# Performance work log

Hardware: AMD Instinct MI355X
Metric: run time of the kernel (lower is better)

Reference implementation:

```python
import jax, jax.numpy as jnp
import numpy as np

N_NODES = 50000
N_EDGES = 800000
IN_FEATS = 128
HIDDEN = 128
OUT_LEN = 128


def setup_inputs() -> dict:
    key = jax.random.key(0)
    ks = jax.random.split(key, 8)
    feat = jax.random.normal(ks[0], (N_NODES, IN_FEATS), dtype=jnp.float32)
    # Glorot-ish init for weights, zeros for bias (DGL GraphConv default)
    def w(k, fi, fo):
        return jax.random.normal(k, (fi, fo), dtype=jnp.float32) / np.sqrt(fi)
    W1 = w(ks[1], IN_FEATS, HIDDEN)
    W2 = w(ks[2], HIDDEN, HIDDEN)
    W3 = w(ks[3], HIDDEN, OUT_LEN)
    b1 = jnp.zeros((HIDDEN,), jnp.float32)
    b2 = jnp.zeros((HIDDEN,), jnp.float32)
    b3 = jnp.zeros((OUT_LEN,), jnp.float32)
    src = jax.random.randint(ks[4], (N_EDGES,), 0, N_NODES, dtype=jnp.int32)
    dst = jax.random.randint(ks[5], (N_EDGES,), 0, N_NODES, dtype=jnp.int32)
    return {"feat": feat, "W1": W1, "b1": b1, "W2": W2, "b2": b2,
            "W3": W3, "b3": b3, "src": src, "dst": dst}


def _degree_norm(idx, n):
    # degree counts, clamped to min 1 (DGL behavior), then ^{-1/2}
    deg = jax.ops.segment_sum(jnp.ones_like(idx, dtype=jnp.float32), idx,
                              num_segments=n)
    return jax.lax.rsqrt(jnp.maximum(deg, 1.0))


def _graph_conv(x, W, b, src, dst, out_norm, in_norm):
    # DGL GraphConv, norm='both':
    # h = D_dst^{-1/2} * segsum_dst( D_src^{-1/2} * x[src] ) @ W + b
    h = x * out_norm[:, None]
    m = jax.ops.segment_sum(h[src], dst, num_segments=x.shape[0])  # [N, d]
    m = m * in_norm[:, None]
    return m @ W + b


def reference(feat, W1, b1, W2, b2, W3, b3, src, dst):
    out_norm = _degree_norm(src, feat.shape[0])  # out-degree norm (source)
    in_norm = _degree_norm(dst, feat.shape[0])   # in-degree norm (dest)
    h = jax.nn.relu(_graph_conv(feat, W1, b1, src, dst, out_norm, in_norm))
    h = jax.nn.relu(_graph_conv(h, W2, b2, src, dst, out_norm, in_norm))
    h = _graph_conv(h, W3, b3, src, dst, out_norm, in_norm)
    # single graph: mean_nodes == mean over all nodes, then squeeze -> [out_len]
    return jnp.mean(h, axis=0)
```

## Files before the change

### kernel.cpp

```cpp
#include <hip/hip_runtime.h>

#define N_NODES 50000
#define N_EDGES 800000
#define F 128
#define SCAN_NB 49
#define CH 64
#define EPC (N_EDGES / CH)
#define HALF 25000
#define QTR 12500
#define BSTRIDE 17
#define AGG_NB (N_NODES / 4)
#define RED_NB 256

typedef __bf16 bf16x8 __attribute__((ext_vector_type(8)));
typedef float  f32x4  __attribute__((ext_vector_type(4)));
typedef float  f32x2  __attribute__((ext_vector_type(2)));

__device__ inline unsigned short f2bf(float f) {
    unsigned u = __float_as_uint(f);
    u += 0x7FFF + ((u >> 16) & 1);
    return (unsigned short)(u >> 16);
}
__device__ inline unsigned packbf2(float a, float b) {
    return (unsigned)f2bf(a) | ((unsigned)f2bf(b) << 16);
}

__device__ inline void fp8x8_to_f32(uint2 u, float* f) {
    f32x2 v0 = __builtin_amdgcn_cvt_pk_f32_fp8(u.x, false);
    f32x2 v1 = __builtin_amdgcn_cvt_pk_f32_fp8(u.x, true);
    f32x2 v2 = __builtin_amdgcn_cvt_pk_f32_fp8(u.y, false);
    f32x2 v3 = __builtin_amdgcn_cvt_pk_f32_fp8(u.y, true);
    f[0] = v0.x; f[1] = v0.y; f[2] = v1.x; f[3] = v1.y;
    f[4] = v2.x; f[5] = v2.y; f[6] = v3.x; f[7] = v3.y;
}
__device__ inline unsigned f32x4_to_fp8(float a, float b, float c, float d) {
    unsigned r = __builtin_amdgcn_cvt_pk_fp8_f32(a, b, 0, false);
    r = __builtin_amdgcn_cvt_pk_fp8_f32(c, d, r, true);
    return r;
}

__global__ __launch_bounds__(1024) void hist_kernel(const int* __restrict__ src,
                                                    const int* __restrict__ dst,
                                                    unsigned short* __restrict__ Hs16,
                                                    unsigned short* __restrict__ Hd16) {
    __shared__ unsigned hist[HALF / 2];
    int bx = blockIdx.x;
    int c = bx >> 2, t = bx & 1, h = (bx >> 1) & 1;
    const int* ids = t ? dst : src;
    unsigned short* H = t ? Hd16 : Hs16;
    int base = h * HALF;
    for (int j = threadIdx.x; j < HALF / 2; j += 1024) hist[j] = 0;
    __syncthreads();
    int e0 = c * EPC;
    for (int e = e0 + threadIdx.x; e < e0 + EPC; e += 1024) {
        int id = ids[e] - base;
        if ((unsigned)id < (unsigned)HALF)
            atomicAdd(&hist[id >> 1], 1u << ((id & 1) * 16));
    }
    __syncthreads();
    for (int j = threadIdx.x; j < HALF / 2; j += 1024)
        *(unsigned*)&H[(size_t)c * N_NODES + base + 2 * j] = hist[j];
}

__global__ __launch_bounds__(1024) void reduceN_kernel(const unsigned short* __restrict__ Hs16,
                                                       const unsigned short* __restrict__ Hd16,
                                                       float* __restrict__ onorm,
                                                       float* __restrict__ inorm,
                                                       int* __restrict__ degd,
                                                       int* __restrict__ bsums) {
    __shared__ int wsum[16];
    int i = blockIdx.x * 1024 + threadIdx.x;
    int dd = 0;
    if (i < N_NODES) {
        int ds = 0;
        for (int c = 0; c < CH; c++) {
            ds += Hs16[(size_t)c * N_NODES + i];
            dd += Hd16[(size_t)c * N_NODES + i];
        }
        onorm[i] = rsqrtf(fmaxf((float)ds, 1.0f));
        inorm[i] = rsqrtf(fmaxf((float)dd, 1.0f));
        degd[i] = dd;
    }
    int v = dd;
#pragma unroll
    for (int off = 32; off; off >>= 1) v += __shfl_down(v, off);
    if ((threadIdx.x & 63) == 0) wsum[threadIdx.x >> 6] = v;
    __syncthreads();
    if (threadIdx.x == 0) {
        int s = 0;
#pragma unroll
        for (int k = 0; k < 16; k++) s += wsum[k];
        bsums[blockIdx.x] = s;
    }
}

__global__ __launch_bounds__(64) void scanB_kernel(const int* __restrict__ blockSums,
                                                   int* __restrict__ blockOffs) {
    int t = threadIdx.x;
    int v = (t < SCAN_NB) ? blockSums[t] : 0;
    int incl = v;
#pragma unroll
    for (int off = 1; off < 64; off <<= 1) {
        int u = __shfl_up(incl, off);
        if (t >= off) incl += u;
    }
    if (t < SCAN_NB) blockOffs[t] = incl - v;
}

__global__ __launch_bounds__(1024) void tq_kernel(const int* __restrict__ src,
                                                  const int* __restrict__ dst,
                                                  const float* __restrict__ inorm,
                                                  float* __restrict__ Tq) {
    __shared__ float a[QTR];
    int bx = blockIdx.x;
    int c = bx >> 2, q = bx & 3;
    int base = q * QTR;
    for (int j = threadIdx.x; j < QTR; j += 1024) a[j] = 0.0f;
    __syncthreads();
    int e0 = c * EPC;
    for (int e = e0 + threadIdx.x; e < e0 + EPC; e += 1024) {
        int s = src[e] - base;
        if ((unsigned)s < (unsigned)QTR)
            atomicAdd(&a[s], inorm[dst[e]]);
    }
    __syncthreads();
    for (int j = threadIdx.x; j < QTR; j += 1024)
        Tq[(size_t)c * N_NODES + base + j] = a[j];
}

__global__ __launch_bounds__(1024) void scanC_kernel(const int* __restrict__ deg,
                                                     const int* __restrict__ blockOffs,
                                                     int* __restrict__ rowst,
                                                     const unsigned short* __restrict__ Hd16,
                                                     int* __restrict__ P,
                                                     const float* __restrict__ Tq,
                                                     float* __restrict__ qt) {
    __shared__ int wsum[16];
    int t = threadIdx.x, lane = t & 63, w = t >> 6;
    int i = blockIdx.x * 1024 + t;
    int v = (i < N_NODES) ? deg[i] : 0;
    int incl = v;
#pragma unroll
    for (int off = 1; off < 64; off <<= 1) {
        int u = __shfl_up(incl, off);
        if (lane >= off) incl += u;
    }
    if (lane == 63) wsum[w] = incl;
    __syncthreads();
    if (t == 0) {
        int s = 0;
#pragma unroll
        for (int k = 0; k < 16; k++) { int x = wsum[k]; wsum[k] = s; s += x; }
    }
    __syncthreads();
    incl += wsum[w] + blockOffs[blockIdx.x];
    if (i < N_NODES) {
        int s = incl - v;
        rowst[i] = s;
        if (i == N_NODES - 1) rowst[N_NODES] = incl;
        float tsum = 0.0f;
        for (int c = 0; c < CH; c++) {
            size_t o = (size_t)c * N_NODES + i;
            P[o] = s; s += Hd16[o];
            tsum += Tq[o];
        }
        qt[i] = tsum;
    }
}

__global__ __launch_bounds__(1024) void scatter2_kernel(const int* __restrict__ src,
                                                        const int* __restrict__ dst,
                                                        const int* __restrict__ P,
                                                        int* __restrict__ esrc) {
    __shared__ int cur[QTR];
    int bx = blockIdx.x;
    int c = bx >> 2, q = bx & 3;
    int base = q * QTR;
    for (int j = threadIdx.x; j < QTR; j += 1024)
        cur[j] = P[(size_t)c * N_NODES + base + j];
    __syncthreads();
    int e0 = c * EPC;
    for (int e = e0 + threadIdx.x; e < e0 + EPC; e += 1024) {
        int d = dst[e] - base;
        if ((unsigned)d < (unsigned)QTR) {
            int pos = atomicAdd(&cur[d], 1);
            esrc[pos] = src[e];
        }
    }
}

__global__ __launch_bounds__(256) void cvt_kernel(const float* __restrict__ x,
                                                  const float* __restrict__ onorm,
                                                  uint2* __restrict__ xq, int n8) {
    int i = blockIdx.x * 256 + threadIdx.x;
    if (i < n8) {
        float w = onorm[i >> 4];
        const float4* xv = (const float4*)x;
        float4 v0 = xv[i * 2], v1 = xv[i * 2 + 1];
        uint2 o;
        o.x = f32x4_to_fp8(v0.x * w, v0.y * w, v0.z * w, v0.w * w);
        o.y = f32x4_to_fp8(v1.x * w, v1.y * w, v1.z * w, v1.w * w);
        xq[i] = o;
    }
}

__global__ __launch_bounds__(128) void wprep_kernel(const float* __restrict__ W1,
                                                    const float* __restrict__ W2,
                                                    unsigned short* __restrict__ Wt_hi,
                                                    unsigned short* __restrict__ Wt_lo) {
    int bx = blockIdx.x;
    int wi = bx >> 7, n = bx & 127;
    const float* W = wi ? W2 : W1;
    int k = threadIdx.x;
    float v = W[k * F + n];
    unsigned short hi = f2bf(v);
    float r = v - __uint_as_float((unsigned)hi << 16);
    size_t o = (size_t)wi * F * F + (size_t)n * F + k;
    Wt_hi[o] = hi;
    Wt_lo[o] = f2bf(r);
}

__global__ __launch_bounds__(256) void agg_csr_kernel(const uint2* __restrict__ xq,
                                                      uint4* __restrict__ mb,
                                                      const int* __restrict__ rowst,
                                                      const int* __restrict__ esrc,
                                                      const float* __restrict__ inorm) {
    int w = threadIdx.x >> 6;
    int lane = threadIdx.x & 63;
    int g = lane >> 4, t = lane & 15;
    int row = blockIdx.x * 4 + w;
    int beg = __builtin_amdgcn_readfirstlane(rowst[row]);
    int end = __builtin_amdgcn_readfirstlane(rowst[row + 1]);
    float acc[8];
#pragma unroll
    for (int k = 0; k < 8; k++) acc[k] = 0.0f;

    for (int e = beg; e < end; e += 16) {
        int ea = min(e + g,      end - 1);
        int eb = min(e + 4 + g,  end - 1);
        int ec = min(e + 8 + g,  end - 1);
        int ed = min(e + 12 + g, end - 1);
        int sa = esrc[ea], sb = esrc[eb], sc = esrc[ec], sd = esrc[ed];
        uint2 ua = xq[(size_t)sa * 16 + t];
        uint2 ub = xq[(size_t)sb * 16 + t];
        uint2 uc = xq[(size_t)sc * 16 + t];
        uint2 ud = xq[(size_t)sd * 16 + t];
        float wa = (e + g      < end) ? 1.0f : 0.0f;
        float wb = (e + 4 + g  < end) ? 1.0f : 0.0f;
        float wc = (e + 8 + g  < end) ? 1.0f : 0.0f;
        float wd = (e + 12 + g < end) ? 1.0f : 0.0f;
        float fa[8], fb[8], fc[8], fd[8];
        fp8x8_to_f32(ua, fa); fp8x8_to_f32(ub, fb);
        fp8x8_to_f32(uc, fc); fp8x8_to_f32(ud, fd);
#pragma unroll
        for (int k = 0; k < 8; k++)
            acc[k] += fa[k] * wa + fb[k] * wb + fc[k] * wc + fd[k] * wd;
    }
#pragma unroll
    for (int k = 0; k < 8; k++) {
        acc[k] += __shfl_xor(acc[k], 16, 64);
        acc[k] += __shfl_xor(acc[k], 32, 64);
    }
    if (g == 0) {
        float inw = inorm[row];
        uint4 o;
        o.x = packbf2(acc[0] * inw, acc[1] * inw);
        o.y = packbf2(acc[2] * inw, acc[3] * inw);
        o.z = packbf2(acc[4] * inw, acc[5] * inw);
        o.w = packbf2(acc[6] * inw, acc[7] * inw);
        mb[(size_t)row * 16 + t] = o;
    }
}

__global__ __launch_bounds__(256) void mfma_gemm_kernel(const unsigned short* __restrict__ A,
                                                        const unsigned short* __restrict__ Wt_hi,
                                                        const unsigned short* __restrict__ Wt_lo,
                                                        const float* __restrict__ bias,
                                                        const float* __restrict__ onorm,
                                                        unsigned char* __restrict__ Y8) {
    __shared__ uint4 sB[F * BSTRIDE];
    int tid = threadIdx.x;
    int w = tid >> 6;
    int lane = tid & 63;
    int quad = lane >> 4, r16 = lane & 15;
    int row0 = blockIdx.x * 64 + w * 16;

    const uint4* Arow = (const uint4*)(A + (size_t)(row0 + r16) * F);
    uint4 a[4];
#pragma unroll
    for (int kk = 0; kk < 4; kk++) a[kk] = Arow[kk * 4 + quad];

    f32x4 acc[8];
#pragma unroll
    for (int t = 0; t < 8; t++) acc[t] = (f32x4){0.f, 0.f, 0.f, 0.f};

    const uint4* G[2] = {(const uint4*)Wt_hi, (const uint4*)Wt_lo};
#pragma unroll
    for (int ph = 0; ph < 2; ph++) {
        if (ph) __syncthreads();
        for (int j = tid; j < F * 16; j += 256)
            sB[(j >> 4) * BSTRIDE + (j & 15)] = G[ph][j];
        __syncthreads();
#pragma unroll
        for (int kk = 0; kk < 4; kk++) {
            bf16x8 av = __builtin_bit_cast(bf16x8, a[kk]);
#pragma unroll
            for (int t = 0; t < 8; t++) {
                bf16x8 bv = __builtin_bit_cast(bf16x8,
                    sB[(t * 16 + r16) * BSTRIDE + kk * 4 + quad]);
                acc[t] = __builtin_amdgcn_mfma_f32_16x16x32_bf16(av, bv, acc[t], 0, 0, 0);
            }
        }
    }

    float onw[4];
#pragma unroll
    for (int reg = 0; reg < 4; reg++) {
        int row = row0 + quad * 4 + reg;
        onw[reg] = (row < N_NODES) ? onorm[row] : 0.0f;
    }
#pragma unroll
    for (int t = 0; t < 8; t++) {
        int col = t * 16 + r16;
        float bb = bias[col];
#pragma unroll
        for (int reg = 0; reg < 4; reg++) {
            int row = row0 + quad * 4 + reg;
            if (row < N_NODES) {
                float v = fmaxf(acc[t][reg] + bb, 0.0f) * onw[reg];
                unsigned p = __builtin_amdgcn_cvt_pk_fp8_f32(v, v, 0, false);
                Y8[(size_t)row * F + col] = (unsigned char)(p & 0xFF);
            }
        }
    }
}

__global__ __launch_bounds__(256) void colsum_kernel(const unsigned short* __restrict__ x8,
                                                     const float* __restrict__ qt,
                                                     float* __restrict__ part2) {
    __shared__ float sP[4][F];
    int tid = threadIdx.x;
    int w = tid >> 6, lane = tid & 63;
    float a0 = 0.0f, a1 = 0.0f;
    for (int r = blockIdx.x * 4 + w; r < N_NODES; r += RED_NB * 4) {
        float q = qt[r];
        unsigned us = x8[(size_t)r * 64 + lane];
        f32x2 v = __builtin_amdgcn_cvt_pk_f32_fp8(us, false);
        a0 += v.x * q; a1 += v.y * q;
    }
    sP[w][lane * 2] = a0; sP[w][lane * 2 + 1] = a1;
    __syncthreads();
    if (tid < F)
        part2[(size_t)blockIdx.x * F + tid] =
            sP[0][tid] + sP[1][tid] + sP[2][tid] + sP[3][tid];
}

__global__ __launch_bounds__(1024) void final_kernel(const float* __restrict__ part2,
                                                     const float* __restrict__ W3,
                                                     const float* __restrict__ b3,
                                                     float* __restrict__ out) {
    __shared__ float sc[8][F];
    int tid = threadIdx.x;
    int col = tid & 127, sl = tid >> 7;
    float acc = 0.0f;
    for (int b = sl; b < RED_NB; b += 8) acc += part2[(size_t)b * F + col];
    sc[sl][col] = acc;
    __syncthreads();
    if (tid < F) {
        float s = 0.0f;
#pragma unroll
        for (int k = 0; k < 8; k++) s += sc[k][tid];
        sc[0][tid] = s * (1.0f / (float)N_NODES);
    }
    __syncthreads();
    if (tid < F) {
        float o = b3[tid];
        for (int k = 0; k < F; k++) o += sc[0][k] * W3[k * F + tid];
        out[tid] = o;
    }
}

extern "C" void kernel_launch(void* const* d_in, const int* in_sizes, int n_in,
                              void* d_out, int out_size, void* d_ws, size_t ws_size,
                              hipStream_t stream) {
    const float* feat = (const float*)d_in[0];
    const float* W1   = (const float*)d_in[1];
    const float* b1   = (const float*)d_in[2];
    const float* W2   = (const float*)d_in[3];
    const float* b2   = (const float*)d_in[4];
    const float* W3   = (const float*)d_in[5];
    const float* b3   = (const float*)d_in[6];
    const int*   src  = (const int*)d_in[7];
    const int*   dst  = (const int*)d_in[8];
    float* out = (float*)d_out;

    char* ws = (char*)d_ws;
    size_t off = 0;
    uint4* mb    = (uint4*)(ws + off); off += (size_t)N_NODES * F * 2;
    float* Tq    = (float*)(ws + off); off += (size_t)CH * N_NODES * 4;
    int*   P     = (int*)  (ws + off); off += (size_t)CH * N_NODES * 4;
    unsigned short* Hs16 = (unsigned short*)(ws + off); off += (size_t)CH * N_NODES * 2;
    unsigned short* Hd16 = (unsigned short*)(ws + off); off += (size_t)CH * N_NODES * 2;
    uint2* xq    = (uint2*)(ws + off); off += (size_t)N_NODES * F;
    uint2* hq    = (uint2*)(ws + off); off += (size_t)N_NODES * F;
    unsigned short* Wt_hi = (unsigned short*)(ws + off); off += 2 * F * F * 2;
    unsigned short* Wt_lo = (unsigned short*)(ws + off); off += 2 * F * F * 2;
    float* part2 = (float*)(ws + off); off += (size_t)RED_NB * F * 4;
    int*   esrc  = (int*)  (ws + off); off += (size_t)N_EDGES * 4;
    float* onorm = (float*)(ws + off); off += N_NODES * 4;
    float* inorm = (float*)(ws + off); off += N_NODES * 4;
    float* qt    = (float*)(ws + off); off += N_NODES * 4;
    int*   degd  = (int*)  (ws + off); off += N_NODES * 4;
    int*   rowst = (int*)  (ws + off); off += (N_NODES + 1) * 4;
    int*   bsums = (int*)  (ws + off); off += 64 * 4;
    int*   boffs = (int*)  (ws + off); off += 64 * 4;

    const int GB = (N_NODES + 63) / 64;

    hist_kernel<<<4 * CH, 1024, 0, stream>>>(src, dst, Hs16, Hd16);
    reduceN_kernel<<<SCAN_NB, 1024, 0, stream>>>(Hs16, Hd16, onorm, inorm, degd, bsums);
    scanB_kernel<<<1, 64, 0, stream>>>(bsums, boffs);
    tq_kernel<<<4 * CH, 1024, 0, stream>>>(src, dst, inorm, Tq);
    scanC_kernel<<<SCAN_NB, 1024, 0, stream>>>(degd, boffs, rowst, Hd16, P, Tq, qt);
    scatter2_kernel<<<4 * CH, 1024, 0, stream>>>(src, dst, P, esrc);

    cvt_kernel<<<(N_NODES * F / 8 + 255) / 256, 256, 0, stream>>>(feat, onorm, xq, N_NODES * F / 8);
    wprep_kernel<<<256, 128, 0, stream>>>(W1, W2, Wt_hi, Wt_lo);

    agg_csr_kernel<<<AGG_NB, 256, 0, stream>>>(xq, mb, rowst, esrc, inorm);
    mfma_gemm_kernel<<<GB, 256, 0, stream>>>((const unsigned short*)mb, Wt_hi, Wt_lo, b1,
                                             onorm, (unsigned char*)hq);
    agg_csr_kernel<<<AGG_NB, 256, 0, stream>>>(hq, mb, rowst, esrc, inorm);
    mfma_gemm_kernel<<<GB, 256, 0, stream>>>((const unsigned short*)mb, Wt_hi + F * F,
                                             Wt_lo + F * F, b2, onorm, (unsigned char*)xq);
    colsum_kernel<<<RED_NB, 256, 0, stream>>>((const unsigned short*)xq, qt, part2);
    final_kernel<<<1, 1024, 0, stream>>>(part2, W3, b3, out);
}
```

Before: 245.9 us.

## Merge prep kernels, fold block scan into scanC, widen aggregation loads, halve chunks

```diff
diff --git a/kernel.cpp b/kernel.cpp
--- a/kernel.cpp
+++ b/kernel.cpp
@@ -4,7 +4,7 @@
 #define N_EDGES 800000
 #define F 128
 #define SCAN_NB 49
-#define CH 64
+#define CH 32
 #define EPC (N_EDGES / CH)
 #define HALF 25000
 #define QTR 12500
@@ -25,13 +25,19 @@
     return (unsigned)f2bf(a) | ((unsigned)f2bf(b) << 16);
 }
 
-__device__ inline void fp8x8_to_f32(uint2 u, float* f) {
+__device__ inline void fp8x16_to_f32(uint4 u, float* f) {
     f32x2 v0 = __builtin_amdgcn_cvt_pk_f32_fp8(u.x, false);
     f32x2 v1 = __builtin_amdgcn_cvt_pk_f32_fp8(u.x, true);
     f32x2 v2 = __builtin_amdgcn_cvt_pk_f32_fp8(u.y, false);
     f32x2 v3 = __builtin_amdgcn_cvt_pk_f32_fp8(u.y, true);
-    f[0] = v0.x; f[1] = v0.y; f[2] = v1.x; f[3] = v1.y;
-    f[4] = v2.x; f[5] = v2.y; f[6] = v3.x; f[7] = v3.y;
+    f32x2 v4 = __builtin_amdgcn_cvt_pk_f32_fp8(u.z, false);
+    f32x2 v5 = __builtin_amdgcn_cvt_pk_f32_fp8(u.z, true);
+    f32x2 v6 = __builtin_amdgcn_cvt_pk_f32_fp8(u.w, false);
+    f32x2 v7 = __builtin_amdgcn_cvt_pk_f32_fp8(u.w, true);
+    f[0] = v0.x;  f[1] = v0.y;  f[2] = v1.x;  f[3] = v1.y;
+    f[4] = v2.x;  f[5] = v2.y;  f[6] = v3.x;  f[7] = v3.y;
+    f[8] = v4.x;  f[9] = v4.y;  f[10] = v5.x; f[11] = v5.y;
+    f[12] = v6.x; f[13] = v6.y; f[14] = v7.x; f[15] = v7.y;
 }
 __device__ inline unsigned f32x4_to_fp8(float a, float b, float c, float d) {
     unsigned r = __builtin_amdgcn_cvt_pk_fp8_f32(a, b, 0, false);
@@ -94,19 +100,6 @@
     }
 }
 
-__global__ __launch_bounds__(64) void scanB_kernel(const int* __restrict__ blockSums,
-                                                   int* __restrict__ blockOffs) {
-    int t = threadIdx.x;
-    int v = (t < SCAN_NB) ? blockSums[t] : 0;
-    int incl = v;
-#pragma unroll
-    for (int off = 1; off < 64; off <<= 1) {
-        int u = __shfl_up(incl, off);
-        if (t >= off) incl += u;
-    }
-    if (t < SCAN_NB) blockOffs[t] = incl - v;
-}
-
 __global__ __launch_bounds__(1024) void tq_kernel(const int* __restrict__ src,
                                                   const int* __restrict__ dst,
                                                   const float* __restrict__ inorm,
@@ -129,7 +122,7 @@
 }
 
 __global__ __launch_bounds__(1024) void scanC_kernel(const int* __restrict__ deg,
-                                                     const int* __restrict__ blockOffs,
+                                                     const int* __restrict__ bsums,
                                                      int* __restrict__ rowst,
                                                      const unsigned short* __restrict__ Hd16,
                                                      int* __restrict__ P,
@@ -149,11 +142,12 @@
     __syncthreads();
     if (t == 0) {
         int s = 0;
+        for (int k = 0; k < (int)blockIdx.x; k++) s += bsums[k];
 #pragma unroll
         for (int k = 0; k < 16; k++) { int x = wsum[k]; wsum[k] = s; s += x; }
     }
     __syncthreads();
-    incl += wsum[w] + blockOffs[blockIdx.x];
+    incl += wsum[w];
     if (i < N_NODES) {
         int s = incl - v;
         rowst[i] = s;
@@ -189,86 +183,86 @@
     }
 }
 
-__global__ __launch_bounds__(256) void cvt_kernel(const float* __restrict__ x,
-                                                  const float* __restrict__ onorm,
-                                                  uint2* __restrict__ xq, int n8) {
-    int i = blockIdx.x * 256 + threadIdx.x;
-    if (i < n8) {
+__global__ __launch_bounds__(256) void prep_kernel(const float* __restrict__ feat,
+                                                   const float* __restrict__ onorm,
+                                                   uint2* __restrict__ xq,
+                                                   const float* __restrict__ W1,
+                                                   const float* __restrict__ W2,
+                                                   unsigned short* __restrict__ Wt_hi,
+                                                   unsigned short* __restrict__ Wt_lo) {
+    int T = gridDim.x * 256;
+    int id0 = blockIdx.x * 256 + threadIdx.x;
+    for (int i = id0; i < N_NODES * F / 8; i += T) {
         float w = onorm[i >> 4];
-        const float4* xv = (const float4*)x;
+        const float4* xv = (const float4*)feat;
         float4 v0 = xv[i * 2], v1 = xv[i * 2 + 1];
         uint2 o;
         o.x = f32x4_to_fp8(v0.x * w, v0.y * w, v0.z * w, v0.w * w);
         o.y = f32x4_to_fp8(v1.x * w, v1.y * w, v1.z * w, v1.w * w);
         xq[i] = o;
     }
-}
-
-__global__ __launch_bounds__(128) void wprep_kernel(const float* __restrict__ W1,
-                                                    const float* __restrict__ W2,
-                                                    unsigned short* __restrict__ Wt_hi,
-                                                    unsigned short* __restrict__ Wt_lo) {
-    int bx = blockIdx.x;
-    int wi = bx >> 7, n = bx & 127;
-    const float* W = wi ? W2 : W1;
-    int k = threadIdx.x;
-    float v = W[k * F + n];
-    unsigned short hi = f2bf(v);
-    float r = v - __uint_as_float((unsigned)hi << 16);
-    size_t o = (size_t)wi * F * F + (size_t)n * F + k;
-    Wt_hi[o] = hi;
-    Wt_lo[o] = f2bf(r);
-}
-
-__global__ __launch_bounds__(256) void agg_csr_kernel(const uint2* __restrict__ xq,
+    for (int i = id0; i < 2 * F * F; i += T) {
+        int wi = i >> 14, rem = i & 16383;
+        int n = rem >> 7, k = rem & 127;
+        const float* W = wi ? W2 : W1;
+        float v = W[k * F + n];
+        unsigned short hi = f2bf(v);
+        float r = v - __uint_as_float((unsigned)hi << 16);
+        size_t o = (size_t)wi * F * F + (size_t)n * F + k;
+        Wt_hi[o] = hi;
+        Wt_lo[o] = f2bf(r);
+    }
+}
+
+__global__ __launch_bounds__(256) void agg_csr_kernel(const uint4* __restrict__ xq4,
                                                       uint4* __restrict__ mb,
                                                       const int* __restrict__ rowst,
                                                       const int* __restrict__ esrc,
                                                       const float* __restrict__ inorm) {
     int w = threadIdx.x >> 6;
     int lane = threadIdx.x & 63;
-    int g = lane >> 4, t = lane & 15;
+    int g = lane >> 3, t = lane & 7;
     int row = blockIdx.x * 4 + w;
     int beg = __builtin_amdgcn_readfirstlane(rowst[row]);
     int end = __builtin_amdgcn_readfirstlane(rowst[row + 1]);
-    float acc[8];
-#pragma unroll
-    for (int k = 0; k < 8; k++) acc[k] = 0.0f;
+    float acc[16];
+#pragma unroll
+    for (int k = 0; k < 16; k++) acc[k] = 0.0f;
 
     for (int e = beg; e < end; e += 16) {
-        int ea = min(e + g,      end - 1);
-        int eb = min(e + 4 + g,  end - 1);
-        int ec = min(e + 8 + g,  end - 1);
-        int ed = min(e + 12 + g, end - 1);
-        int sa = esrc[ea], sb = esrc[eb], sc = esrc[ec], sd = esrc[ed];
-        uint2 ua = xq[(size_t)sa * 16 + t];
-        uint2 ub = xq[(size_t)sb * 16 + t];
-        uint2 uc = xq[(size_t)sc * 16 + t];
-        uint2 ud = xq[(size_t)sd * 16 + t];
-        float wa = (e + g      < end) ? 1.0f : 0.0f;
-        float wb = (e + 4 + g  < end) ? 1.0f : 0.0f;
-        float wc = (e + 8 + g  < end) ? 1.0f : 0.0f;
-        float wd = (e + 12 + g < end) ? 1.0f : 0.0f;
-        float fa[8], fb[8], fc[8], fd[8];
-        fp8x8_to_f32(ua, fa); fp8x8_to_f32(ub, fb);
-        fp8x8_to_f32(uc, fc); fp8x8_to_f32(ud, fd);
-#pragma unroll
-        for (int k = 0; k < 8; k++)
-            acc[k] += fa[k] * wa + fb[k] * wb + fc[k] * wc + fd[k] * wd;
-    }
-#pragma unroll
-    for (int k = 0; k < 8; k++) {
+        int ea = min(e + g,     end - 1);
+        int eb = min(e + 8 + g, end - 1);
+        int sa = esrc[ea], sb = esrc[eb];
+        uint4 ua = xq4[(size_t)sa * 8 + t];
+        uint4 ub = xq4[(size_t)sb * 8 + t];
+        float wa = (e + g     < end) ? 1.0f : 0.0f;
+        float wb = (e + 8 + g < end) ? 1.0f : 0.0f;
+        float fa[16], fb[16];
+        fp8x16_to_f32(ua, fa);
+        fp8x16_to_f32(ub, fb);
+#pragma unroll
+        for (int k = 0; k < 16; k++)
+            acc[k] += fa[k] * wa + fb[k] * wb;
+    }
+#pragma unroll
+    for (int k = 0; k < 16; k++) {
+        acc[k] += __shfl_xor(acc[k], 8, 64);
         acc[k] += __shfl_xor(acc[k], 16, 64);
         acc[k] += __shfl_xor(acc[k], 32, 64);
     }
     if (g == 0) {
         float inw = inorm[row];
-        uint4 o;
-        o.x = packbf2(acc[0] * inw, acc[1] * inw);
-        o.y = packbf2(acc[2] * inw, acc[3] * inw);
-        o.z = packbf2(acc[4] * inw, acc[5] * inw);
-        o.w = packbf2(acc[6] * inw, acc[7] * inw);
-        mb[(size_t)row * 16 + t] = o;
+        uint4 o1, o2;
+        o1.x = packbf2(acc[0] * inw,  acc[1] * inw);
+        o1.y = packbf2(acc[2] * inw,  acc[3] * inw);
+        o1.z = packbf2(acc[4] * inw,  acc[5] * inw);
+        o1.w = packbf2(acc[6] * inw,  acc[7] * inw);
+        o2.x = packbf2(acc[8] * inw,  acc[9] * inw);
+        o2.y = packbf2(acc[10] * inw, acc[11] * inw);
+        o2.z = packbf2(acc[12] * inw, acc[13] * inw);
+        o2.w = packbf2(acc[14] * inw, acc[15] * inw);
+        mb[(size_t)row * 16 + t * 2]     = o1;
+        mb[(size_t)row * 16 + t * 2 + 1] = o2;
     }
 }
 
@@ -413,24 +407,21 @@
     int*   degd  = (int*)  (ws + off); off += N_NODES * 4;
     int*   rowst = (int*)  (ws + off); off += (N_NODES + 1) * 4;
     int*   bsums = (int*)  (ws + off); off += 64 * 4;
-    int*   boffs = (int*)  (ws + off); off += 64 * 4;
 
     const int GB = (N_NODES + 63) / 64;
 
     hist_kernel<<<4 * CH, 1024, 0, stream>>>(src, dst, Hs16, Hd16);
     reduceN_kernel<<<SCAN_NB, 1024, 0, stream>>>(Hs16, Hd16, onorm, inorm, degd, bsums);
-    scanB_kernel<<<1, 64, 0, stream>>>(bsums, boffs);
     tq_kernel<<<4 * CH, 1024, 0, stream>>>(src, dst, inorm, Tq);
-    scanC_kernel<<<SCAN_NB, 1024, 0, stream>>>(degd, boffs, rowst, Hd16, P, Tq, qt);
+    scanC_kernel<<<SCAN_NB, 1024, 0, stream>>>(degd, bsums, rowst, Hd16, P, Tq, qt);
     scatter2_kernel<<<4 * CH, 1024, 0, stream>>>(src, dst, P, esrc);
 
-    cvt_kernel<<<(N_NODES * F / 8 + 255) / 256, 256, 0, stream>>>(feat, onorm, xq, N_NODES * F / 8);
-    wprep_kernel<<<256, 128, 0, stream>>>(W1, W2, Wt_hi, Wt_lo);
-
-    agg_csr_kernel<<<AGG_NB, 256, 0, stream>>>(xq, mb, rowst, esrc, inorm);
+    prep_kernel<<<512, 256, 0, stream>>>(feat, onorm, xq, W1, W2, Wt_hi, Wt_lo);
+
+    agg_csr_kernel<<<AGG_NB, 256, 0, stream>>>((const uint4*)xq, mb, rowst, esrc, inorm);
     mfma_gemm_kernel<<<GB, 256, 0, stream>>>((const unsigned short*)mb, Wt_hi, Wt_lo, b1,
                                              onorm, (unsigned char*)hq);
-    agg_csr_kernel<<<AGG_NB, 256, 0, stream>>>(hq, mb, rowst, esrc, inorm);
+    agg_csr_kernel<<<AGG_NB, 256, 0, stream>>>((const uint4*)hq, mb, rowst, esrc, inorm);
     mfma_gemm_kernel<<<GB, 256, 0, stream>>>((const unsigned short*)mb, Wt_hi + F * F,
                                              Wt_lo + F * F, b2, onorm, (unsigned char*)xq);
     colsum_kernel<<<RED_NB, 256, 0, stream>>>((const unsigned short*)xq, qt, part2);
```

Result: slower. 289.2 us (+17.6%).
